# Performance work log

Measured on AMD Instinct MI355X. Metric: run time of the kernel, lower is better.

The kernel has to match this reference:

```python
import jax, jax.numpy as jnp
import numpy as np
from jax import lax

S, V, DW = 2048, 50000, 400     # seq_len, word vocab, word emb dim
CV, DC = 8, 32                  # casing vocab / dim
PV, DP = 50, 64                 # POS vocab / dim
H, C = 768, 13                  # lstm hidden (per direction), num tag classes
DIN = DW + DC + DP              # 496 lstm input dim


def setup_inputs() -> dict:
    key = jax.random.key(0)
    ks = jax.random.split(key, 18)
    r = lambda k, sh, s=0.02: (jax.random.normal(k, sh) * s).astype(jnp.float32)
    return {
        "x": jax.random.randint(ks[0], (S,), 0, V),
        "casing": jax.random.randint(ks[1], (S,), 0, CV),
        "pos": jax.random.randint(ks[2], (S,), 0, PV),
        "word_emb": r(ks[3], (V, DW)),
        "casing_emb": r(ks[4], (CV, DC)),
        "pos_emb": r(ks[5], (PV, DP)),
        "Wih_f": r(ks[6], (4 * H, DIN)),
        "Whh_f": r(ks[7], (4 * H, H)),
        "b_f": jnp.zeros((4 * H,), jnp.float32),
        "Wih_b": r(ks[8], (4 * H, DIN)),
        "Whh_b": r(ks[9], (4 * H, H)),
        "b_b": jnp.zeros((4 * H,), jnp.float32),
        "Wc": r(ks[10], (C, 2 * H)),
        "bc": jnp.zeros((C,), jnp.float32),
        "start_trans": r(ks[11], (C,), 0.1),
        "end_trans": r(ks[12], (C,), 0.1),
        "trans": r(ks[13], (C, C), 0.1),
        "h0": jnp.zeros((2, H), jnp.float32),
        "c0": jnp.zeros((2, H), jnp.float32),
    }


def _lstm(xg, Whh, h0, c0):
    # xg: (S, 4H) precomputed input-to-hidden gates; PyTorch gate order i,f,g,o
    def step(carry, g_in):
        h, c = carry
        g = g_in + h @ Whh.T
        i, f, gg, o = jnp.split(g, 4)
        c = jax.nn.sigmoid(f) * c + jax.nn.sigmoid(i) * jnp.tanh(gg)
        h = jax.nn.sigmoid(o) * jnp.tanh(c)
        return (h, c), h
    _, hs = lax.scan(step, (h0, c0), xg)
    return hs  # (S, H)


def reference(x, casing, pos, word_emb, casing_emb, pos_emb,
              Wih_f, Whh_f, b_f, Wih_b, Whh_b, b_b, Wc, bc,
              start_trans, end_trans, trans, h0, c0):
    # embedding concat -> (S, DIN)
    emb = jnp.concatenate([word_emb[x], casing_emb[casing], pos_emb[pos]], axis=-1)
    # weight-dropped LSTM (eval mode: DropConnect identity), bidirectional
    hs_f = _lstm(emb @ Wih_f.T + b_f, Whh_f, h0[0], c0[0])
    hs_b = _lstm((emb @ Wih_b.T + b_b)[::-1], Whh_b, h0[1], c0[1])[::-1]
    o = jnp.concatenate([hs_f, hs_b], axis=-1) @ Wc.T + bc  # (S, C)
    tag_scores = jax.nn.log_softmax(o, axis=1)
    # CRF Viterbi decode (torchcrf-style), batch of 1 (the unsqueeze(0))
    score0 = start_trans + tag_scores[0]
    def vstep(score, em):
        cand = score[:, None] + trans            # (prev C, next C)
        bp = jnp.argmax(cand, axis=0)
        return jnp.max(cand, axis=0) + em, bp
    score, bps = lax.scan(vstep, score0, tag_scores[1:])
    last = jnp.argmax(score + end_trans)
    def back(tag, bp):
        prev = bp[tag]
        return prev, prev
    _, prevs = lax.scan(back, last, bps[::-1])
    tags = jnp.concatenate([prevs[::-1], last[None]])  # (S,) best path
    return tag_scores, tags
```

## Files before the change

### kernel.cpp

```cpp
#include <hip/hip_runtime.h>
#include <hip/hip_bf16.h>


#define SEQ  2048
#define DINW 496
#define HDIM 768
#define G4   3072
#define CDIM 13
#define NWG  48
#define JPW  16
#define DATA_SPIN (1u << 14)

__device__ __forceinline__ float sigf(float x) { return 1.0f / (1.0f + __expf(-x)); }
__device__ __forceinline__ float tanhf_fast(float x) {
    float ax = fabsf(x);
    float e  = __expf(-2.0f * ax);
    float t  = (1.0f - e) / (1.0f + e);
    return copysignf(t, x);
}

__global__ __launch_bounds__(256) void k_gemm_xg(
    const int* __restrict__ x, const int* __restrict__ casing, const int* __restrict__ pos,
    const float* __restrict__ we, const float* __restrict__ ce, const float* __restrict__ pe,
    const float* __restrict__ Wih_f, const float* __restrict__ b_f,
    const float* __restrict__ Wih_b, const float* __restrict__ b_b,
    __hip_bfloat16* __restrict__ xg_f, __hip_bfloat16* __restrict__ xg_b)
{
    __shared__ float As[16][132];
    __shared__ float Bs[16][132];
    int dir = blockIdx.z;
    const float* B    = dir ? Wih_b : Wih_f;
    const float* bias = dir ? b_b   : b_f;
    __hip_bfloat16* C = dir ? xg_b  : xg_f;
    int n0 = blockIdx.x * 128, m0 = blockIdx.y * 128;
    int tid = threadIdx.x;
    int r  = tid >> 1, cb = (tid & 1) * 8;
    int tx = tid & 15, ty = tid >> 4;

    int m = m0 + r;
    const float* arow_w = we + (size_t)x[m] * 400;
    const float* arow_c = ce + (size_t)casing[m] * 32;
    const float* arow_p = pe + (size_t)pos[m] * 64;
    const float* brow   = B + (size_t)(n0 + r) * DINW;

    float acc[8][8] = {};
    for (int k0 = 0; k0 < DINW; k0 += 16) {
        int c0 = k0 + cb;
        float4 a0, a1, b0, b1;
        if (c0 < 400)      a0 = *(const float4*)(arow_w + c0);
        else if (c0 < 432) a0 = *(const float4*)(arow_c + (c0 - 400));
        else               a0 = *(const float4*)(arow_p + (c0 - 432));
        int c4 = c0 + 4;
        if (c4 < 400)      a1 = *(const float4*)(arow_w + c4);
        else if (c4 < 432) a1 = *(const float4*)(arow_c + (c4 - 400));
        else               a1 = *(const float4*)(arow_p + (c4 - 432));
        b0 = *(const float4*)(brow + c0);
        b1 = *(const float4*)(brow + c4);
        __syncthreads();
        As[cb + 0][r] = a0.x; As[cb + 1][r] = a0.y; As[cb + 2][r] = a0.z; As[cb + 3][r] = a0.w;
        As[cb + 4][r] = a1.x; As[cb + 5][r] = a1.y; As[cb + 6][r] = a1.z; As[cb + 7][r] = a1.w;
        Bs[cb + 0][r] = b0.x; Bs[cb + 1][r] = b0.y; Bs[cb + 2][r] = b0.z; Bs[cb + 3][r] = b0.w;
        Bs[cb + 4][r] = b1.x; Bs[cb + 5][r] = b1.y; Bs[cb + 6][r] = b1.z; Bs[cb + 7][r] = b1.w;
        __syncthreads();
        #pragma unroll
        for (int k = 0; k < 16; k++) {
            float4 av0 = *(const float4*)&As[k][ty * 8];
            float4 av1 = *(const float4*)&As[k][ty * 8 + 4];
            float4 bv0 = *(const float4*)&Bs[k][tx * 8];
            float4 bv1 = *(const float4*)&Bs[k][tx * 8 + 4];
            float aa[8] = {av0.x, av0.y, av0.z, av0.w, av1.x, av1.y, av1.z, av1.w};
            float bb[8] = {bv0.x, bv0.y, bv0.z, bv0.w, bv1.x, bv1.y, bv1.z, bv1.w};
            #pragma unroll
            for (int i = 0; i < 8; i++)
                #pragma unroll
                for (int jj = 0; jj < 8; jj++)
                    acc[i][jj] += aa[i] * bb[jj];
        }
    }
    float4 bs0 = *(const float4*)(bias + n0 + tx * 8);
    float4 bs1 = *(const float4*)(bias + n0 + tx * 8 + 4);
    float bb8[8] = {bs0.x, bs0.y, bs0.z, bs0.w, bs1.x, bs1.y, bs1.z, bs1.w};
    #pragma unroll
    for (int i = 0; i < 8; i++) {
        int row = m0 + ty * 8 + i;
        union { __hip_bfloat16 h[4]; ushort4 u; } c0v, c1v;
        #pragma unroll
        for (int jj = 0; jj < 4; jj++) {
            c0v.h[jj] = __float2bfloat16(acc[i][jj] + bb8[jj]);
            c1v.h[jj] = __float2bfloat16(acc[i][jj + 4] + bb8[jj + 4]);
        }
        *(ushort4*)(C + (size_t)row * G4 + n0 + tx * 8)     = c0v.u;
        *(ushort4*)(C + (size_t)row * G4 + n0 + tx * 8 + 4) = c1v.u;
    }
}

__global__ __launch_bounds__(1024) void k_lstm(
    const __hip_bfloat16* __restrict__ xg_f, const __hip_bfloat16* __restrict__ xg_b,
    const float* __restrict__ Whh_f, const float* __restrict__ Whh_b,
    const float* __restrict__ h0, const float* __restrict__ c0v,
    float* __restrict__ hs_f, float* __restrict__ hs_b,
    unsigned* __restrict__ msg, unsigned* __restrict__ abortw)
{
    __shared__ float hbuf[2][HDIM];
    __shared__ unsigned sdead;

    int wg = blockIdx.x;
    int dir = wg & 1, slot = wg >> 1;
    const __hip_bfloat16* xg = dir ? xg_b : xg_f;
    const float* Whh = dir ? Whh_b : Whh_f;
    float* hs        = dir ? hs_b  : hs_f;
    unsigned* mdir = msg + (size_t)dir * 2 * HDIM;

    int tid = threadIdx.x, lane = tid & 63, wv = tid >> 6;
    int q = lane >> 4, gl = lane & 15;
    int j = slot * JPW + wv;

    float w[48];
    const float* wr = Whh + (size_t)(q * HDIM + j) * HDIM;
    #pragma unroll
    for (int m = 0; m < 12; m++) {
        float4 f4 = *(const float4*)(wr + gl * 4 + m * 64);
        w[m * 4 + 0] = f4.x; w[m * 4 + 1] = f4.y;
        w[m * 4 + 2] = f4.z; w[m * 4 + 3] = f4.w;
    }
    float cst = c0v[dir * HDIM + j];

    if (tid == 0) sdead = 0;

    for (int t = 0; t < SEQ; t++) {
        int xrow = dir ? (SEQ - 1 - t) : t;
        const __hip_bfloat16* xga = xg + (size_t)xrow * G4 + j;
        float xv0 = __bfloat162float(xga[0]);
        float xv1 = __bfloat162float(xga[HDIM]);
        float xv2 = __bfloat162float(xga[2 * HDIM]);
        float xv3 = __bfloat162float(xga[3 * HDIM]);

        int par = (t & 1) ^ 1;

        if (wv < 2) {
            int base = wv * 6;
            if (t == 0) {
                #pragma unroll
                for (int m = 0; m < 6; m++)
                    hbuf[1][(base + m) * 64 + lane] = h0[dir * HDIM + (base + m) * 64 + lane];
            } else {
                const unsigned* g = mdir + (size_t)par * HDIM;
                unsigned vals[6];
                unsigned fresh = 0, rounds = 0;
                bool dead = false;
                for (;;) {
                    #pragma unroll
                    for (int m = 0; m < 6; m++)
                        if (!(fresh & (1u << m)))
                            vals[m] = __hip_atomic_load(&g[(base + m) * 64 + lane],
                                        __ATOMIC_RELAXED, __HIP_MEMORY_SCOPE_AGENT);
                    #pragma unroll
                    for (int m = 0; m < 6; m++)
                        if ((vals[m] >> 16) == (unsigned)t) fresh |= (1u << m);
                    if (__all(fresh == 0x3Fu)) break;
                    unsigned ab = __hip_atomic_load(abortw,
                                    __ATOMIC_RELAXED, __HIP_MEMORY_SCOPE_AGENT);
                    if (ab || ++rounds >= DATA_SPIN) { dead = true; break; }
                }
                #pragma unroll
                for (int m = 0; m < 6; m++) {
                    union { unsigned u; float f; } cvt;
                    cvt.u = (vals[m] & 0xFFFFu) << 16;
                    hbuf[par][(base + m) * 64 + lane] = cvt.f;
                }
                if (dead && lane == 0) {
                    __hip_atomic_store(abortw, 1u,
                                       __ATOMIC_RELAXED, __HIP_MEMORY_SCOPE_AGENT);
                    sdead = 1;
                }
            }
        }

        __syncthreads();
        if (sdead) break;

        float acc = 0.f;
        #pragma unroll
        for (int m = 0; m < 12; m++) {
            float4 f4 = *(const float4*)&hbuf[par][gl * 4 + m * 64];
            acc += w[m * 4 + 0] * f4.x + w[m * 4 + 1] * f4.y
                 + w[m * 4 + 2] * f4.z + w[m * 4 + 3] * f4.w;
        }
        acc += __shfl_xor(acc, 1);
        acc += __shfl_xor(acc, 2);
        acc += __shfl_xor(acc, 4);
        acc += __shfl_xor(acc, 8);
        float si = __shfl(acc, 0),  sf = __shfl(acc, 16);
        float sg = __shfl(acc, 32), so = __shfl(acc, 48);

        float gi = sigf(xv0 + si), gf = sigf(xv1 + sf);
        float gg = tanhf_fast(xv2 + sg), go = sigf(xv3 + so);
        cst = gf * cst + gi * gg;
        float h = go * tanhf_fast(cst);

        if (lane == 0) {
            union { __hip_bfloat16 b; unsigned short u; } cv;
            cv.b = __float2bfloat16(h);
            unsigned word = ((unsigned)(t + 1) << 16) | (unsigned)cv.u;
            __hip_atomic_store(&mdir[(size_t)(t & 1) * HDIM + j], word,
                               __ATOMIC_RELAXED, __HIP_MEMORY_SCOPE_AGENT);
            int hrow = dir ? (SEQ - 1 - t) : t;
            hs[(size_t)hrow * HDIM + j] = h;
        }
        __syncthreads();
    }
}

__global__ __launch_bounds__(256) void k_head(
    const float* __restrict__ hs_f, const float* __restrict__ hs_b,
    const float* __restrict__ Wc, const float* __restrict__ bc,
    float* __restrict__ out)
{
    int tid = threadIdx.x, lane = tid & 63, wv = tid >> 6;
    int row = blockIdx.x * 4 + wv;
    const float* src = (lane < 32) ? (hs_f + (size_t)row * HDIM + lane * 24)
                                   : (hs_b + (size_t)row * HDIM + (lane - 32) * 24);
    float hvv[24];
    #pragma unroll
    for (int k = 0; k < 6; k++) {
        float4 f4 = *(const float4*)(src + k * 4);
        hvv[k * 4 + 0] = f4.x; hvv[k * 4 + 1] = f4.y;
        hvv[k * 4 + 2] = f4.z; hvv[k * 4 + 3] = f4.w;
    }
    int off = (lane < 32) ? lane * 24 : 768 + (lane - 32) * 24;
    float o[13];
    #pragma unroll
    for (int n = 0; n < CDIM; n++) {
        const float* wr2 = Wc + (size_t)n * 1536 + off;
        float s0 = 0.f, s1 = 0.f, s2 = 0.f, s3 = 0.f;
        #pragma unroll
        for (int k = 0; k < 6; k++) {
            float4 w4 = *(const float4*)(wr2 + k * 4);
            s0 += w4.x * hvv[k * 4 + 0];
            s1 += w4.y * hvv[k * 4 + 1];
            s2 += w4.z * hvv[k * 4 + 2];
            s3 += w4.w * hvv[k * 4 + 3];
        }
        o[n] = (s0 + s1) + (s2 + s3);
    }
    #pragma unroll
    for (int n = 0; n < CDIM; n++) {
        #pragma unroll
        for (int d = 1; d < 64; d <<= 1) o[n] += __shfl_xor(o[n], d);
        o[n] += bc[n];
    }
    float m = o[0];
    #pragma unroll
    for (int n = 1; n < CDIM; n++) m = fmaxf(m, o[n]);
    float sum = 0.f;
    #pragma unroll
    for (int n = 0; n < CDIM; n++) sum += __expf(o[n] - m);
    float ls = m + __logf(sum);
    if (lane == 0) {
        #pragma unroll
        for (int n = 0; n < CDIM; n++) out[(size_t)row * CDIM + n] = o[n] - ls;
    }
}

__global__ __launch_bounds__(64) void k_viterbi(
    const float* __restrict__ ts, const float* __restrict__ st,
    const float* __restrict__ en, const float* __restrict__ tr,
    float* __restrict__ tags_out)
{
    __shared__ unsigned char bp[SEQ - 1][16];
    __shared__ unsigned char path[SEQ];
    int n = threadIdx.x;
    bool act = n < CDIM;
    float trn[CDIM];
    #pragma unroll
    for (int p = 0; p < CDIM; p++) trn[p] = act ? tr[p * CDIM + n] : -1e30f;
    float score = act ? (st[n] + ts[n]) : -1e30f;

    for (int s = 1; s < SEQ; s++) {
        float em = act ? ts[(size_t)s * CDIM + n] : 0.f;
        float sp[CDIM];
        #pragma unroll
        for (int p = 0; p < CDIM; p++) sp[p] = __shfl(score, p);
        float best = -1e30f; int arg = 0;
        #pragma unroll
        for (int p = 0; p < CDIM; p++) {
            float v = sp[p] + trn[p];
            if (v > best) { best = v; arg = p; }
        }
        score = best + em;
        if (act) bp[s - 1][n] = (unsigned char)arg;
    }
    float fin = act ? (score + en[n]) : -1e30f;
    float fv[CDIM];
    #pragma unroll
    for (int p = 0; p < CDIM; p++) fv[p] = __shfl(fin, p);
    __syncthreads();
    if (n == 0) {
        float best = -1e30f; int last = 0;
        #pragma unroll
        for (int p = 0; p < CDIM; p++) { if (fv[p] > best) { best = fv[p]; last = p; } }
        int cur = last;
        path[SEQ - 1] = (unsigned char)cur;
        for (int s = SEQ - 2; s >= 0; s--) { cur = bp[s][cur]; path[s] = (unsigned char)cur; }
    }
    __syncthreads();
    for (int i = n; i < SEQ; i += 64) tags_out[i] = (float)path[i];
}

__global__ void k_zero(float* p, int n) {
    int i = blockIdx.x * 256 + threadIdx.x;
    if (i < n) p[i] = 0.f;
}

extern "C" void kernel_launch(void* const* d_in, const int* in_sizes, int n_in,
                              void* d_out, int out_size, void* d_ws, size_t ws_size,
                              hipStream_t stream)
{
    const int*   x      = (const int*)d_in[0];
    const int*   casing = (const int*)d_in[1];
    const int*   pos    = (const int*)d_in[2];
    const float* we     = (const float*)d_in[3];
    const float* ce     = (const float*)d_in[4];
    const float* pe     = (const float*)d_in[5];
    const float* Wih_f  = (const float*)d_in[6];
    const float* Whh_f  = (const float*)d_in[7];
    const float* b_f    = (const float*)d_in[8];
    const float* Wih_b  = (const float*)d_in[9];
    const float* Whh_b  = (const float*)d_in[10];
    const float* b_b    = (const float*)d_in[11];
    const float* Wc     = (const float*)d_in[12];
    const float* bc     = (const float*)d_in[13];
    const float* strt   = (const float*)d_in[14];
    const float* endt   = (const float*)d_in[15];
    const float* trans  = (const float*)d_in[16];
    const float* h0     = (const float*)d_in[17];
    const float* c0     = (const float*)d_in[18];

    const size_t need = 37761028;
    if (ws_size < need) {
        k_zero<<<(out_size + 255) / 256, 256, 0, stream>>>((float*)d_out, out_size);
        return;
    }
    char* wsb = (char*)d_ws;
    float* hs_f = (float*)(wsb);
    float* hs_b = (float*)(wsb + 6291456);
    __hip_bfloat16* xg_f = (__hip_bfloat16*)(wsb + 12582912);
    __hip_bfloat16* xg_b = (__hip_bfloat16*)(wsb + 25165824);
    unsigned* msg = (unsigned*)(wsb + 37748736);
    unsigned* abortw = (unsigned*)(wsb + 37761024);

    hipMemsetAsync(msg, 0, 12288 + 4, stream);

    k_gemm_xg<<<dim3(G4 / 128, SEQ / 128, 2), 256, 0, stream>>>(
        x, casing, pos, we, ce, pe, Wih_f, b_f, Wih_b, b_b, xg_f, xg_b);
    k_lstm<<<2 * NWG, 1024, 0, stream>>>(
        xg_f, xg_b, Whh_f, Whh_b, h0, c0, hs_f, hs_b, msg, abortw);
    k_head<<<SEQ / 4, 256, 0, stream>>>(hs_f, hs_b, Wc, bc, (float*)d_out);
    k_viterbi<<<1, 64, 0, stream>>>(
        (const float*)d_out, strt, endt, trans, (float*)d_out + (size_t)SEQ * CDIM);
}
```

Baseline: 6.051 ms.

## Replace LSTM step barriers with LDS flag handoff; stage head weights in LDS

Inside the persistent LSTM kernel, the two __syncthreads per timestep are replaced by per-parity LDS flags. The two loader waves publish a flag once they have written the step's hidden state, and the compute waves spin on it with acquire loads. This lets waves run ahead without a full workgroup barrier. The head kernel now stages Wc in shared memory and processes 16 rows per block instead of 4, cutting redundant global weight reads. The flag scheme depends on double-buffered hbuf parity, so a fast wave could race ahead into a buffer that slow waves are still reading, and spin loops also compete for issue slots.

```diff
diff --git a/kernel.cpp b/kernel.cpp
--- a/kernel.cpp
+++ b/kernel.cpp
@@ -10,6 +10,8 @@
 #define NWG  48
 #define JPW  16
 #define DATA_SPIN (1u << 14)
+#define DEADFLAG 0x7FFFFFFFu
+#define DEADBIT  0x40000000u
 
 __device__ __forceinline__ float sigf(float x) { return 1.0f / (1.0f + __expf(-x)); }
 __device__ __forceinline__ float tanhf_fast(float x) {
@@ -102,7 +104,7 @@
     unsigned* __restrict__ msg, unsigned* __restrict__ abortw)
 {
     __shared__ float hbuf[2][HDIM];
-    __shared__ unsigned sdead;
+    __shared__ unsigned lflag[2][2];
 
     int wg = blockIdx.x;
     int dir = wg & 1, slot = wg >> 1;
@@ -125,7 +127,8 @@
     }
     float cst = c0v[dir * HDIM + j];
 
-    if (tid == 0) sdead = 0;
+    if (tid < 4) ((unsigned*)lflag)[tid] = 0;
+    __syncthreads();
 
     for (int t = 0; t < SEQ; t++) {
         int xrow = dir ? (SEQ - 1 - t) : t;
@@ -139,6 +142,7 @@
 
         if (wv < 2) {
             int base = wv * 6;
+            bool dead = false;
             if (t == 0) {
                 #pragma unroll
                 for (int m = 0; m < 6; m++)
@@ -147,7 +151,6 @@
                 const unsigned* g = mdir + (size_t)par * HDIM;
                 unsigned vals[6];
                 unsigned fresh = 0, rounds = 0;
-                bool dead = false;
                 for (;;) {
                     #pragma unroll
                     for (int m = 0; m < 6; m++)
@@ -168,16 +171,28 @@
                     cvt.u = (vals[m] & 0xFFFFu) << 16;
                     hbuf[par][(base + m) * 64 + lane] = cvt.f;
                 }
-                if (dead && lane == 0) {
+            }
+            if (lane == 0) {
+                if (dead) {
                     __hip_atomic_store(abortw, 1u,
                                        __ATOMIC_RELAXED, __HIP_MEMORY_SCOPE_AGENT);
-                    sdead = 1;
+                    __hip_atomic_store(&lflag[0][wv], DEADFLAG,
+                                       __ATOMIC_RELEASE, __HIP_MEMORY_SCOPE_WORKGROUP);
+                    __hip_atomic_store(&lflag[1][wv], DEADFLAG,
+                                       __ATOMIC_RELEASE, __HIP_MEMORY_SCOPE_WORKGROUP);
+                } else {
+                    __hip_atomic_store(&lflag[par][wv], (unsigned)(t + 1),
+                                       __ATOMIC_RELEASE, __HIP_MEMORY_SCOPE_WORKGROUP);
                 }
             }
         }
 
-        __syncthreads();
-        if (sdead) break;
+        unsigned f0, f1;
+        do { f0 = __hip_atomic_load(&lflag[par][0], __ATOMIC_ACQUIRE,
+                                    __HIP_MEMORY_SCOPE_WORKGROUP); } while (f0 < (unsigned)(t + 1));
+        do { f1 = __hip_atomic_load(&lflag[par][1], __ATOMIC_ACQUIRE,
+                                    __HIP_MEMORY_SCOPE_WORKGROUP); } while (f1 < (unsigned)(t + 1));
+        if ((f0 | f1) & DEADBIT) break;
 
         float acc = 0.f;
         #pragma unroll
@@ -207,7 +222,6 @@
             int hrow = dir ? (SEQ - 1 - t) : t;
             hs[(size_t)hrow * HDIM + j] = h;
         }
-        __syncthreads();
     }
 }
 
@@ -216,49 +230,61 @@
     const float* __restrict__ Wc, const float* __restrict__ bc,
     float* __restrict__ out)
 {
-    int tid = threadIdx.x, lane = tid & 63, wv = tid >> 6;
-    int row = blockIdx.x * 4 + wv;
-    const float* src = (lane < 32) ? (hs_f + (size_t)row * HDIM + lane * 24)
-                                   : (hs_b + (size_t)row * HDIM + (lane - 32) * 24);
-    float hvv[24];
-    #pragma unroll
-    for (int k = 0; k < 6; k++) {
-        float4 f4 = *(const float4*)(src + k * 4);
-        hvv[k * 4 + 0] = f4.x; hvv[k * 4 + 1] = f4.y;
-        hvv[k * 4 + 2] = f4.z; hvv[k * 4 + 3] = f4.w;
-    }
+    __shared__ float wcs[CDIM][1536];
+    __shared__ float bcs[CDIM];
+    int tid = threadIdx.x;
+    for (int i = tid; i < CDIM * 1536; i += 256) {
+        int n = i / 1536;
+        wcs[n][i - n * 1536] = Wc[i];
+    }
+    if (tid < CDIM) bcs[tid] = bc[tid];
+    __syncthreads();
+
+    int lane = tid & 63, wv = tid >> 6;
     int off = (lane < 32) ? lane * 24 : 768 + (lane - 32) * 24;
-    float o[13];
-    #pragma unroll
-    for (int n = 0; n < CDIM; n++) {
-        const float* wr2 = Wc + (size_t)n * 1536 + off;
-        float s0 = 0.f, s1 = 0.f, s2 = 0.f, s3 = 0.f;
+    for (int rr = 0; rr < 4; rr++) {
+        int row = blockIdx.x * 16 + wv * 4 + rr;
+        const float* src = (lane < 32) ? (hs_f + (size_t)row * HDIM + lane * 24)
+                                       : (hs_b + (size_t)row * HDIM + (lane - 32) * 24);
+        float hvv[24];
         #pragma unroll
         for (int k = 0; k < 6; k++) {
-            float4 w4 = *(const float4*)(wr2 + k * 4);
-            s0 += w4.x * hvv[k * 4 + 0];
-            s1 += w4.y * hvv[k * 4 + 1];
-            s2 += w4.z * hvv[k * 4 + 2];
-            s3 += w4.w * hvv[k * 4 + 3];
-        }
-        o[n] = (s0 + s1) + (s2 + s3);
-    }
-    #pragma unroll
-    for (int n = 0; n < CDIM; n++) {
-        #pragma unroll
-        for (int d = 1; d < 64; d <<= 1) o[n] += __shfl_xor(o[n], d);
-        o[n] += bc[n];
-    }
-    float m = o[0];
-    #pragma unroll
-    for (int n = 1; n < CDIM; n++) m = fmaxf(m, o[n]);
-    float sum = 0.f;
-    #pragma unroll
-    for (int n = 0; n < CDIM; n++) sum += __expf(o[n] - m);
-    float ls = m + __logf(sum);
-    if (lane == 0) {
-        #pragma unroll
-        for (int n = 0; n < CDIM; n++) out[(size_t)row * CDIM + n] = o[n] - ls;
+            float4 f4 = *(const float4*)(src + k * 4);
+            hvv[k * 4 + 0] = f4.x; hvv[k * 4 + 1] = f4.y;
+            hvv[k * 4 + 2] = f4.z; hvv[k * 4 + 3] = f4.w;
+        }
+        float o[CDIM];
+        #pragma unroll
+        for (int n = 0; n < CDIM; n++) {
+            const float* wr2 = &wcs[n][off];
+            float s0 = 0.f, s1 = 0.f, s2 = 0.f, s3 = 0.f;
+            #pragma unroll
+            for (int k = 0; k < 6; k++) {
+                float4 w4 = *(const float4*)(wr2 + k * 4);
+                s0 += w4.x * hvv[k * 4 + 0];
+                s1 += w4.y * hvv[k * 4 + 1];
+                s2 += w4.z * hvv[k * 4 + 2];
+                s3 += w4.w * hvv[k * 4 + 3];
+            }
+            o[n] = (s0 + s1) + (s2 + s3);
+        }
+        #pragma unroll
+        for (int n = 0; n < CDIM; n++) {
+            #pragma unroll
+            for (int d = 1; d < 64; d <<= 1) o[n] += __shfl_xor(o[n], d);
+            o[n] += bcs[n];
+        }
+        float m = o[0];
+        #pragma unroll
+        for (int n = 1; n < CDIM; n++) m = fmaxf(m, o[n]);
+        float sum = 0.f;
+        #pragma unroll
+        for (int n = 0; n < CDIM; n++) sum += __expf(o[n] - m);
+        float ls = m + __logf(sum);
+        if (lane == 0) {
+            #pragma unroll
+            for (int n = 0; n < CDIM; n++) out[(size_t)row * CDIM + n] = o[n] - ls;
+        }
     }
 }
 
@@ -355,7 +381,7 @@
         x, casing, pos, we, ce, pe, Wih_f, b_f, Wih_b, b_b, xg_f, xg_b);
     k_lstm<<<2 * NWG, 1024, 0, stream>>>(
         xg_f, xg_b, Whh_f, Whh_b, h0, c0, hs_f, hs_b, msg, abortw);
-    k_head<<<SEQ / 4, 256, 0, stream>>>(hs_f, hs_b, Wc, bc, (float*)d_out);
+    k_head<<<SEQ / 16, 256, 0, stream>>>(hs_f, hs_b, Wc, bc, (float*)d_out);
     k_viterbi<<<1, 64, 0, stream>>>(
         (const float*)d_out, strt, endt, trans, (float*)d_out + (size_t)SEQ * CDIM);
 }
```

Result: slower. 9.271 ms (+53.2%).

## Halve LSTM workgroups with two hidden units per wave and bf16-packed weights

Applied to the files above, without the earlier changes.

The persistent LSTM kernel now runs 24 workgroups per direction instead of 48. Each wave computes two hidden units and keeps both weight rows in registers packed as bf16 pairs, which keeps register pressure roughly the same. Fewer workgroups means fewer participants in the per-step global flag exchange. The cost is double the per-wave compute on the critical path and lower weight precision. Separately, the classifier head stages Wc in shared memory and processes 16 rows per block.

```diff
diff --git a/kernel.cpp b/kernel.cpp
--- a/kernel.cpp
+++ b/kernel.cpp
@@ -7,8 +7,8 @@
 #define HDIM 768
 #define G4   3072
 #define CDIM 13
-#define NWG  48
-#define JPW  16
+#define NWG  24
+#define JPW  32
 #define DATA_SPIN (1u << 14)
 
 __device__ __forceinline__ float sigf(float x) { return 1.0f / (1.0f + __expf(-x)); }
@@ -17,6 +17,11 @@
     float e  = __expf(-2.0f * ax);
     float t  = (1.0f - e) / (1.0f + e);
     return copysignf(t, x);
+}
+__device__ __forceinline__ unsigned pack_bf16(float a, float b) {
+    union { __hip_bfloat16 h; unsigned short u; } x, y;
+    x.h = __float2bfloat16(a); y.h = __float2bfloat16(b);
+    return (unsigned)x.u | ((unsigned)y.u << 16);
 }
 
 __global__ __launch_bounds__(256) void k_gemm_xg(
@@ -113,27 +118,40 @@
 
     int tid = threadIdx.x, lane = tid & 63, wv = tid >> 6;
     int q = lane >> 4, gl = lane & 15;
-    int j = slot * JPW + wv;
-
-    float w[48];
-    const float* wr = Whh + (size_t)(q * HDIM + j) * HDIM;
-    #pragma unroll
-    for (int m = 0; m < 12; m++) {
-        float4 f4 = *(const float4*)(wr + gl * 4 + m * 64);
-        w[m * 4 + 0] = f4.x; w[m * 4 + 1] = f4.y;
-        w[m * 4 + 2] = f4.z; w[m * 4 + 3] = f4.w;
-    }
-    float cst = c0v[dir * HDIM + j];
+    int jA = slot * JPW + wv;
+    int jB = jA + 16;
+
+    unsigned wA[24], wB[24];
+    {
+        const float* wrA = Whh + (size_t)(q * HDIM + jA) * HDIM;
+        const float* wrB = Whh + (size_t)(q * HDIM + jB) * HDIM;
+        #pragma unroll
+        for (int m = 0; m < 12; m++) {
+            float4 a = *(const float4*)(wrA + gl * 4 + m * 64);
+            float4 b = *(const float4*)(wrB + gl * 4 + m * 64);
+            wA[m * 2 + 0] = pack_bf16(a.x, a.y);
+            wA[m * 2 + 1] = pack_bf16(a.z, a.w);
+            wB[m * 2 + 0] = pack_bf16(b.x, b.y);
+            wB[m * 2 + 1] = pack_bf16(b.z, b.w);
+        }
+    }
+    float cstA = c0v[dir * HDIM + jA];
+    float cstB = c0v[dir * HDIM + jB];
 
     if (tid == 0) sdead = 0;
 
     for (int t = 0; t < SEQ; t++) {
         int xrow = dir ? (SEQ - 1 - t) : t;
-        const __hip_bfloat16* xga = xg + (size_t)xrow * G4 + j;
-        float xv0 = __bfloat162float(xga[0]);
-        float xv1 = __bfloat162float(xga[HDIM]);
-        float xv2 = __bfloat162float(xga[2 * HDIM]);
-        float xv3 = __bfloat162float(xga[3 * HDIM]);
+        const __hip_bfloat16* xgaA = xg + (size_t)xrow * G4 + jA;
+        const __hip_bfloat16* xgaB = xg + (size_t)xrow * G4 + jB;
+        float xvA0 = __bfloat162float(xgaA[0]);
+        float xvA1 = __bfloat162float(xgaA[HDIM]);
+        float xvA2 = __bfloat162float(xgaA[2 * HDIM]);
+        float xvA3 = __bfloat162float(xgaA[3 * HDIM]);
+        float xvB0 = __bfloat162float(xgaB[0]);
+        float xvB1 = __bfloat162float(xgaB[HDIM]);
+        float xvB2 = __bfloat162float(xgaB[2 * HDIM]);
+        float xvB3 = __bfloat162float(xgaB[3 * HDIM]);
 
         int par = (t & 1) ^ 1;
 
@@ -179,33 +197,54 @@
         __syncthreads();
         if (sdead) break;
 
-        float acc = 0.f;
+        float accA = 0.f, accB = 0.f;
         #pragma unroll
         for (int m = 0; m < 12; m++) {
             float4 f4 = *(const float4*)&hbuf[par][gl * 4 + m * 64];
-            acc += w[m * 4 + 0] * f4.x + w[m * 4 + 1] * f4.y
-                 + w[m * 4 + 2] * f4.z + w[m * 4 + 3] * f4.w;
-        }
-        acc += __shfl_xor(acc, 1);
-        acc += __shfl_xor(acc, 2);
-        acc += __shfl_xor(acc, 4);
-        acc += __shfl_xor(acc, 8);
-        float si = __shfl(acc, 0),  sf = __shfl(acc, 16);
-        float sg = __shfl(acc, 32), so = __shfl(acc, 48);
-
-        float gi = sigf(xv0 + si), gf = sigf(xv1 + sf);
-        float gg = tanhf_fast(xv2 + sg), go = sigf(xv3 + so);
-        cst = gf * cst + gi * gg;
-        float h = go * tanhf_fast(cst);
+            unsigned a0 = wA[m * 2], a1 = wA[m * 2 + 1];
+            unsigned b0 = wB[m * 2], b1 = wB[m * 2 + 1];
+            accA += __uint_as_float(a0 << 16)          * f4.x
+                  + __uint_as_float(a0 & 0xFFFF0000u)  * f4.y
+                  + __uint_as_float(a1 << 16)          * f4.z
+                  + __uint_as_float(a1 & 0xFFFF0000u)  * f4.w;
+            accB += __uint_as_float(b0 << 16)          * f4.x
+                  + __uint_as_float(b0 & 0xFFFF0000u)  * f4.y
+                  + __uint_as_float(b1 << 16)          * f4.z
+                  + __uint_as_float(b1 & 0xFFFF0000u)  * f4.w;
+        }
+        #pragma unroll
+        for (int d = 1; d < 16; d <<= 1) {
+            accA += __shfl_xor(accA, d);
+            accB += __shfl_xor(accB, d);
+        }
+        float siA = __shfl(accA, 0),  sfA = __shfl(accA, 16);
+        float sgA = __shfl(accA, 32), soA = __shfl(accA, 48);
+        float siB = __shfl(accB, 0),  sfB = __shfl(accB, 16);
+        float sgB = __shfl(accB, 32), soB = __shfl(accB, 48);
+
+        float giA = sigf(xvA0 + siA), gfA = sigf(xvA1 + sfA);
+        float ggA = tanhf_fast(xvA2 + sgA), goA = sigf(xvA3 + soA);
+        cstA = gfA * cstA + giA * ggA;
+        float hA = goA * tanhf_fast(cstA);
+
+        float giB = sigf(xvB0 + siB), gfB = sigf(xvB1 + sfB);
+        float ggB = tanhf_fast(xvB2 + sgB), goB = sigf(xvB3 + soB);
+        cstB = gfB * cstB + giB * ggB;
+        float hB = goB * tanhf_fast(cstB);
 
         if (lane == 0) {
-            union { __hip_bfloat16 b; unsigned short u; } cv;
-            cv.b = __float2bfloat16(h);
-            unsigned word = ((unsigned)(t + 1) << 16) | (unsigned)cv.u;
-            __hip_atomic_store(&mdir[(size_t)(t & 1) * HDIM + j], word,
+            union { __hip_bfloat16 b; unsigned short u; } cvA, cvB;
+            cvA.b = __float2bfloat16(hA);
+            cvB.b = __float2bfloat16(hB);
+            unsigned wordA = ((unsigned)(t + 1) << 16) | (unsigned)cvA.u;
+            unsigned wordB = ((unsigned)(t + 1) << 16) | (unsigned)cvB.u;
+            __hip_atomic_store(&mdir[(size_t)(t & 1) * HDIM + jA], wordA,
+                               __ATOMIC_RELAXED, __HIP_MEMORY_SCOPE_AGENT);
+            __hip_atomic_store(&mdir[(size_t)(t & 1) * HDIM + jB], wordB,
                                __ATOMIC_RELAXED, __HIP_MEMORY_SCOPE_AGENT);
             int hrow = dir ? (SEQ - 1 - t) : t;
-            hs[(size_t)hrow * HDIM + j] = h;
+            hs[(size_t)hrow * HDIM + jA] = hA;
+            hs[(size_t)hrow * HDIM + jB] = hB;
         }
         __syncthreads();
     }
@@ -216,49 +255,61 @@
     const float* __restrict__ Wc, const float* __restrict__ bc,
     float* __restrict__ out)
 {
-    int tid = threadIdx.x, lane = tid & 63, wv = tid >> 6;
-    int row = blockIdx.x * 4 + wv;
-    const float* src = (lane < 32) ? (hs_f + (size_t)row * HDIM + lane * 24)
-                                   : (hs_b + (size_t)row * HDIM + (lane - 32) * 24);
-    float hvv[24];
-    #pragma unroll
-    for (int k = 0; k < 6; k++) {
-        float4 f4 = *(const float4*)(src + k * 4);
-        hvv[k * 4 + 0] = f4.x; hvv[k * 4 + 1] = f4.y;
-        hvv[k * 4 + 2] = f4.z; hvv[k * 4 + 3] = f4.w;
-    }
+    __shared__ float wcs[CDIM][1536];
+    __shared__ float bcs[CDIM];
+    int tid = threadIdx.x;
+    for (int i = tid; i < CDIM * 1536; i += 256) {
+        int n = i / 1536;
+        wcs[n][i - n * 1536] = Wc[i];
+    }
+    if (tid < CDIM) bcs[tid] = bc[tid];
+    __syncthreads();
+
+    int lane = tid & 63, wv = tid >> 6;
     int off = (lane < 32) ? lane * 24 : 768 + (lane - 32) * 24;
-    float o[13];
-    #pragma unroll
-    for (int n = 0; n < CDIM; n++) {
-        const float* wr2 = Wc + (size_t)n * 1536 + off;
-        float s0 = 0.f, s1 = 0.f, s2 = 0.f, s3 = 0.f;
+    for (int rr = 0; rr < 4; rr++) {
+        int row = blockIdx.x * 16 + wv * 4 + rr;
+        const float* src = (lane < 32) ? (hs_f + (size_t)row * HDIM + lane * 24)
+                                       : (hs_b + (size_t)row * HDIM + (lane - 32) * 24);
+        float hvv[24];
         #pragma unroll
         for (int k = 0; k < 6; k++) {
-            float4 w4 = *(const float4*)(wr2 + k * 4);
-            s0 += w4.x * hvv[k * 4 + 0];
-            s1 += w4.y * hvv[k * 4 + 1];
-            s2 += w4.z * hvv[k * 4 + 2];
-            s3 += w4.w * hvv[k * 4 + 3];
-        }
-        o[n] = (s0 + s1) + (s2 + s3);
-    }
-    #pragma unroll
-    for (int n = 0; n < CDIM; n++) {
-        #pragma unroll
-        for (int d = 1; d < 64; d <<= 1) o[n] += __shfl_xor(o[n], d);
-        o[n] += bc[n];
-    }
-    float m = o[0];
-    #pragma unroll
-    for (int n = 1; n < CDIM; n++) m = fmaxf(m, o[n]);
-    float sum = 0.f;
-    #pragma unroll
-    for (int n = 0; n < CDIM; n++) sum += __expf(o[n] - m);
-    float ls = m + __logf(sum);
-    if (lane == 0) {
-        #pragma unroll
-        for (int n = 0; n < CDIM; n++) out[(size_t)row * CDIM + n] = o[n] - ls;
+            float4 f4 = *(const float4*)(src + k * 4);
+            hvv[k * 4 + 0] = f4.x; hvv[k * 4 + 1] = f4.y;
+            hvv[k * 4 + 2] = f4.z; hvv[k * 4 + 3] = f4.w;
+        }
+        float o[CDIM];
+        #pragma unroll
+        for (int n = 0; n < CDIM; n++) {
+            const float* wr2 = &wcs[n][off];
+            float s0 = 0.f, s1 = 0.f, s2 = 0.f, s3 = 0.f;
+            #pragma unroll
+            for (int k = 0; k < 6; k++) {
+                float4 w4 = *(const float4*)(wr2 + k * 4);
+                s0 += w4.x * hvv[k * 4 + 0];
+                s1 += w4.y * hvv[k * 4 + 1];
+                s2 += w4.z * hvv[k * 4 + 2];
+                s3 += w4.w * hvv[k * 4 + 3];
+            }
+            o[n] = (s0 + s1) + (s2 + s3);
+        }
+        #pragma unroll
+        for (int n = 0; n < CDIM; n++) {
+            #pragma unroll
+            for (int d = 1; d < 64; d <<= 1) o[n] += __shfl_xor(o[n], d);
+            o[n] += bcs[n];
+        }
+        float m = o[0];
+        #pragma unroll
+        for (int n = 1; n < CDIM; n++) m = fmaxf(m, o[n]);
+        float sum = 0.f;
+        #pragma unroll
+        for (int n = 0; n < CDIM; n++) sum += __expf(o[n] - m);
+        float ls = m + __logf(sum);
+        if (lane == 0) {
+            #pragma unroll
+            for (int n = 0; n < CDIM; n++) out[(size_t)row * CDIM + n] = o[n] - ls;
+        }
     }
 }
 
@@ -355,7 +406,7 @@
         x, casing, pos, we, ce, pe, Wih_f, b_f, Wih_b, b_b, xg_f, xg_b);
     k_lstm<<<2 * NWG, 1024, 0, stream>>>(
         xg_f, xg_b, Whh_f, Whh_b, h0, c0, hs_f, hs_b, msg, abortw);
-    k_head<<<SEQ / 4, 256, 0, stream>>>(hs_f, hs_b, Wc, bc, (float*)d_out);
+    k_head<<<SEQ / 16, 256, 0, stream>>>(hs_f, hs_b, Wc, bc, (float*)d_out);
     k_viterbi<<<1, 64, 0, stream>>>(
         (const float*)d_out, strt, endt, trans, (float*)d_out + (size_t)SEQ * CDIM);
 }
```

Measured after the change: 9.687 ms. +60.1%, slower.
